# Kernel tuning notes

Hardware: AMD Instinct MI355X
Metric: run time of the kernel (lower is better)

Reference implementation:

```python
import jax, jax.numpy as jnp
import numpy as np

H, W = 480, 640
B = 4
P = 10          # number of accumulated flow passes (num_flows = 1)
N = 400000      # events per batch element
TREF = 1.0
TS_SCALING = 1.0
SPAT_W = 1.0
TEMP_W = 1.0


def _corners(loc):
    """loc: [M,2] (y,x) float -> flattened corner idx [4M] int32, bilinear weights [4M].
    Corner order: TL, TR, BL, BR (blocks of M), matching pol_mask repeat(1,4,1) layout.
    Out-of-grid corners get zero weight; indices are clamped in-range."""
    ty = jnp.floor(loc[:, 0:1])
    lx = jnp.floor(loc[:, 1:2])
    cs = jnp.concatenate([
        jnp.concatenate([ty, lx], 1),
        jnp.concatenate([ty, lx + 1.0], 1),
        jnp.concatenate([ty + 1.0, lx], 1),
        jnp.concatenate([ty + 1.0, lx + 1.0], 1)], axis=0)  # [4M,2]
    w = jnp.maximum(0.0, 1.0 - jnp.abs(jnp.tile(loc, (4, 1)) - cs))
    weights = w[:, 0] * w[:, 1]
    inb = ((cs[:, 0] >= 0) & (cs[:, 0] <= H - 1) &
           (cs[:, 1] >= 0) & (cs[:, 1] <= W - 1))
    weights = weights * inb.astype(weights.dtype)
    idx = (jnp.clip(cs[:, 0], 0, H - 1) * W + jnp.clip(cs[:, 1], 0, W - 1)).astype(jnp.int32)
    return idx, weights


def setup_inputs() -> dict:
    key = jax.random.key(0)
    k1, k2, k3, k4, k5 = jax.random.split(key, 5)
    scale = jnp.array([H - 1.0, W - 1.0], dtype=jnp.float32)
    warped_events = jax.random.uniform(k1, (B, N, 2), dtype=jnp.float32) * scale
    pos = jax.random.bernoulli(k2, 0.5, (B, N)).astype(jnp.float32)
    pos4 = jnp.tile(pos, (1, 4))                                   # [B,4N]
    pol_mask = jnp.stack([pos4, 1.0 - pos4], axis=-1)              # [B,4N,2]
    ts = jax.random.uniform(k3, (B, N, 1), dtype=jnp.float32)
    ts_list = jnp.tile(ts, (1, 4, 1))                              # [B,4N,1]
    flow_x = jax.random.normal(k4, (B, P, H, W), dtype=jnp.float32) * 3.0
    flow_y = jax.random.normal(k5, (B, P, H, W), dtype=jnp.float32) * 3.0
    return {"warped_events": warped_events, "pol_mask": pol_mask,
            "ts_list": ts_list, "flow_x": flow_x, "flow_y": flow_y}


def reference(warped_events, pol_mask, ts_list, flow_x, flow_y):
    f32 = flow_x.dtype
    # ---- iwe_formatting: bilinear scatter-add of warped events ----
    idx, weights = jax.vmap(_corners)(warped_events)               # [B,4N], [B,4N]
    norm_ts = 1.0 - jnp.abs(TREF - ts_list[..., 0]) / TS_SCALING   # [B,4N]

    def scat(i, w):
        return jnp.zeros(H * W, w.dtype).at[i].add(w)

    def img(w):
        return jax.vmap(scat)(idx, w).reshape(B, 1, H, W)

    iwe = jnp.concatenate([img(weights * pol_mask[:, :, 0]),
                           img(weights * pol_mask[:, :, 1])], axis=1)          # [B,2,H,W]
    iwe_ts = jnp.concatenate([img(weights * norm_ts * pol_mask[:, :, 0]),
                              img(weights * norm_ts * pol_mask[:, :, 1])], axis=1)

    # ---- focus_loss ----
    ts2 = iwe_ts.reshape(B, 2, -1)
    fl = jnp.sum(ts2[:, 0] ** 2, axis=1) + jnp.sum(ts2[:, 1] ** 2, axis=1)
    nz = (jnp.sum(iwe, axis=1) != 0).reshape(B, -1)
    fl = fl / (jnp.sum(nz, axis=1) + 1e-9)
    focus = jnp.sum(fl)

    # ---- flow_temporal_smoothing: warp grid by flow[j], gather flow[j+1] ----
    grid = jnp.stack(jnp.meshgrid(jnp.arange(H, dtype=f32),
                                  jnp.arange(W, dtype=f32), indexing='ij'), 0)  # [2,H,W] (y,x)
    flow = jnp.stack([flow_y[:, :-1], flow_x[:, :-1]], axis=2)                  # [B,P-1,2,H,W]
    loc = (grid[None, None] + flow).reshape(B, P - 1, 2, H * W).transpose(0, 1, 3, 2)  # [B,P-1,HW,2]
    m = ((loc[..., 0] >= 0) & (loc[..., 0] <= H - 1) &
         (loc[..., 1] >= 0) & (loc[..., 1] <= W - 1)).astype(f32)

    def samp(fx, fy, l):
        # fx, fy: [H,W]; l: [HW,2] -> sampled (y,x) flow [HW,2]
        i, w = _corners(l)
        sx = (fx.reshape(-1)[i] * w).reshape(4, -1).sum(0)
        sy = (fy.reshape(-1)[i] * w).reshape(4, -1).sum(0)
        return jnp.stack([sy, sx], axis=-1)

    wf = jax.vmap(jax.vmap(samp))(flow_x[:, 1:], flow_y[:, 1:], loc)            # [B,P-1,HW,2]
    ff = flow.reshape(B, P - 1, 2, H * W).transpose(0, 1, 3, 2)
    dt = jnp.sum(jnp.sqrt((ff - wf) ** 2 + 1e-9), axis=-1)                      # [B,P-1,HW]
    lt = jnp.sum(dt * m, axis=-1) / (jnp.sum(m, axis=-1) + 1e-9)                # [B,P-1]
    temporal = TEMP_W * jnp.sum(jnp.sum(lt, axis=1) / (P - 1))                  # num_flows = 1

    # ---- flow_spatial_smoothing: Charbonnier on 4 neighbor directions ----
    def charb(a):
        return jnp.sqrt(a ** 2 + 1e-6)

    dx = charb(flow_x[..., :-1] - flow_x[..., 1:]) + charb(flow_y[..., :-1] - flow_y[..., 1:])
    dy = charb(flow_x[:, :, :-1, :] - flow_x[:, :, 1:, :]) + charb(flow_y[:, :, :-1, :] - flow_y[:, :, 1:, :])
    ddr = charb(flow_x[:, :, :-1, :-1] - flow_x[:, :, 1:, 1:]) + charb(flow_y[:, :, :-1, :-1] - flow_y[:, :, 1:, 1:])
    dur = charb(flow_x[:, :, 1:, :-1] - flow_x[:, :, :-1, 1:]) + charb(flow_y[:, :, 1:, :-1] - flow_y[:, :, :-1, 1:])
    mm = lambda t: t.reshape(B, P, -1).mean(2).mean(1)
    spatial = SPAT_W * jnp.sum((mm(dx) + mm(dy) + mm(ddr) + mm(dur)) / 4.0)

    return focus + temporal + spatial
```

## Files before the change

### kernel.cpp

```cpp
#include <hip/hip_runtime.h>

#define BB 4
#define PP 10
#define NN 400000
#define HH 480
#define WW 640
constexpr int HW    = HH * WW;
constexpr int NXB   = HW / 256;
constexpr int TLW   = 64, TLH = 16;
constexpr int NXT   = (WW / TLW) * (HH / TLH);
constexpr int NTILE = NXT * BB * PP;
constexpr int CHUNK = NTILE / 8;
constexpr int EVB   = (BB * NN + NTILE - 1) / NTILE;

constexpr int WR = 41, WC = 89, WCP = 90;

constexpr int QW = WW / 2, QH = HH / 2, QN = QW * QH;
constexpr size_t IMG_QUADS = (size_t)4 * BB * 2 * QN;

constexpr float SCALE     = 1024.0f;
constexpr float INV_SCALE = 1.0f / 1024.0f;

constexpr int PF_V = 0;
constexpr int PF_N = PF_V + BB * NXB;
constexpr int PT_D = PF_N + BB * NXB;
constexpr int PT_M = PT_D + BB * (PP-1) * NXT * 4;
constexpr int PS   = PT_M + BB * (PP-1) * NXT * 4;
constexpr int NPART = PS + BB * PP * NXT * 4;


__device__ __forceinline__ float fsq(float a) { return __builtin_amdgcn_sqrtf(a); }
__device__ __forceinline__ float charb(float a) { return fsq(fmaf(a, a, 1e-6f)); }

__device__ __forceinline__ void waveSum3(float& a, float& b, float& c) {
    #pragma unroll
    for (int off = 32; off > 0; off >>= 1) {
        a += __shfl_down(a, off, 64);
        b += __shfl_down(b, off, 64);
        c += __shfl_down(c, off, 64);
    }
}

__device__ __forceinline__ float blockSum256(float v, float* smem) {
    #pragma unroll
    for (int off = 32; off > 0; off >>= 1)
        v += __shfl_down(v, off, 64);
    int lane = threadIdx.x & 63;
    int wid  = threadIdx.x >> 6;
    if (lane == 0) smem[wid] = v;
    __syncthreads();
    float r = 0.f;
    if (threadIdx.x == 0) r = smem[0] + smem[1] + smem[2] + smem[3];
    __syncthreads();
    return r;
}

__device__ __forceinline__ void scatter_one(int e,
                                            const float2* __restrict__ we,
                                            const float* __restrict__ pol,
                                            const float* __restrict__ tsl,
                                            unsigned long long* __restrict__ img) {
    int b = e / NN;
    int m = e - b * NN;
    float2 c = we[e];
    float y = c.x, x = c.y;
    float pm0 = pol[((size_t)b * 4 * NN + m) * 2];
    float ts  = tsl[(size_t)b * 4 * NN + m];
    float nts = 1.0f - fabsf(1.0f - ts);
    float tyf = fminf(fmaxf(floorf(y), 0.f), (float)(HH - 2));
    float lxf = fminf(fmaxf(floorf(x), 0.f), (float)(WW - 2));
    float fy_ = y - tyf, fx_ = x - lxf;
    float gy = 1.f - fy_, gx = 1.f - fx_;
    float s = nts * SCALE;
    unsigned long long wTL = (unsigned int)(gy * gx * s + 0.5f);
    unsigned long long wTR = (unsigned int)(gy * fx_ * s + 0.5f);
    unsigned long long wBL = (unsigned int)(fy_ * gx * s + 0.5f);
    unsigned long long wBR = (unsigned int)(fy_ * fx_ * s + 0.5f);
    unsigned long long val = wTL | (wTR << 16) | (wBL << 32) | (wBR << 48);
    int ty = (int)tyf, lx = (int)lxf;
    int pi = ((ty & 1) << 1) | (lx & 1);
    int pl = (pm0 > 0.5f) ? 0 : 1;
    size_t wi = ((size_t)((pi * BB + b) * 2 + pl)) * QN + (ty >> 1) * QW + (lx >> 1);
    atomicAdd(&img[wi], val);
}


__global__ __launch_bounds__(256)
void fused_kernel(const float2* __restrict__ we,
                  const float* __restrict__ pol,
                  const float* __restrict__ tsl,
                  const float* __restrict__ FX, const float* __restrict__ FY,
                  unsigned long long* __restrict__ img,
                  float* __restrict__ part) {
    __shared__ float sfx[WR][WCP];
    __shared__ float sfy[WR][WCP];
    int w = blockIdx.x;
    int t = threadIdx.x;

    int l  = (w & 7) * CHUNK + (w >> 3);
    int bp = l / NXT;
    int xb = l - bp * NXT;
    int b2 = bp / PP;
    int j  = bp - b2 * PP;
    int x0 = (xb % (WW / TLW)) * TLW;
    int y0 = (xb / (WW / TLW)) * TLH;
    const float* fx = FX + (size_t)bp * HW;
    const float* fy = FY + (size_t)bp * HW;
    const float* gx1 = fx + HW;
    const float* gy1 = fy + HW;
    bool hasT = (j < PP - 1);

    int wy0 = y0 - 12, wx0 = x0 - 12;
    if (hasT) {
        for (int idx = t; idx < WR * WC; idx += 256) {
            int r = idx / WC, c = idx - r * WC;
            int gy = min(max(wy0 + r, 0), HH - 1);
            int gc = min(max(wx0 + c, 0), WW - 1);
            sfx[r][c] = gx1[gy * WW + gc];
            sfy[r][c] = gy1[gy * WW + gc];
        }
    }

    int ypx = y0 + (t >> 4);
    int xpx = x0 + (t & 15) * 4;
    int p0  = ypx * WW + xpx;
    float4 vx = *(const float4*)(fx + p0);
    float4 vy = *(const float4*)(fy + p0);
    bool yin  = (ypx + 1 < HH);
    bool xend = (xpx == WW - 4);
    float4 bx4 = make_float4(0.f, 0.f, 0.f, 0.f), by4 = bx4;
    float vxr = 0.f, vyr = 0.f, bxr = 0.f, byr = 0.f;
    if (yin) {
        bx4 = *(const float4*)(fx + p0 + WW);
        by4 = *(const float4*)(fy + p0 + WW);
    }
    if (!xend) { vxr = fx[p0 + 4]; vyr = fy[p0 + 4]; }
    if (yin && !xend) { bxr = fx[p0 + WW + 4]; byr = fy[p0 + WW + 4]; }

    constexpr float cdx = 1.0f / ((float)HH * (WW - 1) * 4.0f * PP);
    constexpr float cdy = 1.0f / ((float)(HH - 1) * WW * 4.0f * PP);
    constexpr float cdd = 1.0f / ((float)(HH - 1) * (WW - 1) * 4.0f * PP);

    float acc = 0.f;
    acc += (charb(vx.x - vx.y) + charb(vy.x - vy.y)) * cdx;
    acc += (charb(vx.y - vx.z) + charb(vy.y - vy.z)) * cdx;
    acc += (charb(vx.z - vx.w) + charb(vy.z - vy.w)) * cdx;
    if (!xend) acc += (charb(vx.w - vxr) + charb(vy.w - vyr)) * cdx;
    if (yin) {
        acc += (charb(vx.x - bx4.x) + charb(vy.x - by4.x)) * cdy;
        acc += (charb(vx.y - bx4.y) + charb(vy.y - by4.y)) * cdy;
        acc += (charb(vx.z - bx4.z) + charb(vy.z - by4.z)) * cdy;
        acc += (charb(vx.w - bx4.w) + charb(vy.w - by4.w)) * cdy;
        acc += (charb(vx.x - bx4.y) + charb(vy.x - by4.y)) * cdd;
        acc += (charb(vx.y - bx4.z) + charb(vy.y - by4.z)) * cdd;
        acc += (charb(vx.z - bx4.w) + charb(vy.z - by4.w)) * cdd;
        acc += (charb(bx4.x - vx.y) + charb(by4.x - vy.y)) * cdd;
        acc += (charb(bx4.y - vx.z) + charb(by4.y - vy.z)) * cdd;
        acc += (charb(bx4.z - vx.w) + charb(by4.z - vy.w)) * cdd;
        if (!xend) {
            acc += (charb(vx.w - bxr) + charb(vy.w - byr)) * cdd;
            acc += (charb(bx4.w - vxr) + charb(by4.w - vyr)) * cdd;
        }
    }

    float td = 0.f, tm = 0.f;
    if (hasT) {
        __syncthreads();
        float ax[4] = {vx.x, vx.y, vx.z, vx.w};
        float ay[4] = {vy.x, vy.y, vy.z, vy.w};
        #pragma unroll
        for (int i = 0; i < 4; ++i) {
            float ly  = (float)ypx + ay[i];
            float lx2 = (float)(xpx + i) + ax[i];
            bool m = (ly >= 0.f) && (ly <= (float)(HH - 1)) &&
                     (lx2 >= 0.f) && (lx2 <= (float)(WW - 1));
            if (m) {
                tm += 1.f;
                float tyf = fminf(fmaxf(floorf(ly),  0.f), (float)(HH - 2));
                float txf = fminf(fmaxf(floorf(lx2), 0.f), (float)(WW - 2));
                int ity = (int)tyf, itx = (int)txf;
                float fyy = ly - tyf, fxx = lx2 - txf;
                float gyy = 1.f - fyy, gxx = 1.f - fxx;
                float x00, x01, x10, x11, y00, y01, y10, y11;
                if (ity >= wy0 && ity <= wy0 + WR - 2 &&
                    itx >= wx0 && itx <= wx0 + WC - 2) {
                    int r = ity - wy0, c = itx - wx0;
                    x00 = sfx[r][c];     x01 = sfx[r][c + 1];
                    x10 = sfx[r + 1][c]; x11 = sfx[r + 1][c + 1];
                    y00 = sfy[r][c];     y01 = sfy[r][c + 1];
                    y10 = sfy[r + 1][c]; y11 = sfy[r + 1][c + 1];
                } else {
                    int pix = ity * WW + itx;
                    x00 = gx1[pix];      x01 = gx1[pix + 1];
                    x10 = gx1[pix + WW]; x11 = gx1[pix + WW + 1];
                    y00 = gy1[pix];      y01 = gy1[pix + 1];
                    y10 = gy1[pix + WW]; y11 = gy1[pix + WW + 1];
                }
                float sx = gyy * (gxx * x00 + fxx * x01) + fyy * (gxx * x10 + fxx * x11);
                float sy = gyy * (gxx * y00 + fxx * y01) + fyy * (gxx * y10 + fxx * y11);
                float dy_ = ay[i] - sy;
                float dx_ = ax[i] - sx;
                td += fsq(fmaf(dy_, dy_, 1e-9f)) + fsq(fmaf(dx_, dx_, 1e-9f));
            }
        }
    }

    __builtin_amdgcn_sched_barrier(0);
    int e = w * EVB + t;
    if (t < EVB && e < BB * NN)
        scatter_one(e, we, pol, tsl, img);
    __builtin_amdgcn_sched_barrier(0);

    waveSum3(acc, td, tm);
    if ((t & 63) == 0) {
        int wid = t >> 6;
        part[PS + (bp * NXT + xb) * 4 + wid] = acc;
        if (hasT) {
            int bj = b2 * (PP - 1) + j;
            part[PT_D + (bj * NXT + xb) * 4 + wid] = td;
            part[PT_M + (bj * NXT + xb) * 4 + wid] = tm;
        }
    }
}


__global__ __launch_bounds__(256)
void focus_kernel(const unsigned long long* __restrict__ img,
                  float* __restrict__ part) {
    __shared__ float sm[8];
    int b = blockIdx.y;
    int p = blockIdx.x * 256 + threadIdx.x;
    int y = p / WW;
    int x = p - y * WW;
    unsigned int sp = 0, sn = 0;
    #pragma unroll
    for (int dy = 0; dy < 2; ++dy) {
        #pragma unroll
        for (int dx = 0; dx < 2; ++dx) {
            int ty = y - dy, lx = x - dx;
            if (ty < 0 || lx < 0 || ty > HH - 2 || lx > WW - 2) continue;
            int pi = ((ty & 1) << 1) | (lx & 1);
            size_t base = ((size_t)(pi * BB + b) * 2) * QN + (ty >> 1) * QW + (lx >> 1);
            int sh = 16 * ((dy << 1) | dx);
            sp += (unsigned int)((img[base]      >> sh) & 0xFFFFull);
            sn += (unsigned int)((img[base + QN] >> sh) & 0xFFFFull);
        }
    }
    float tp = (float)sp * INV_SCALE;
    float tn = (float)sn * INV_SCALE;
    float v  = tp * tp + tn * tn;
    float nz = ((sp | sn) != 0u) ? 1.f : 0.f;
    float sv  = blockSum256(v, sm);
    float snz = blockSum256(nz, sm + 4);
    if (threadIdx.x == 0) {
        part[PF_V + b * NXB + blockIdx.x] = sv;
        part[PF_N + b * NXB + blockIdx.x] = snz;
    }
}


__global__ __launch_bounds__(256)
void reduce_kernel(const float* __restrict__ part, float* __restrict__ seg) {
    __shared__ float sm[4];
    int s = blockIdx.x;
    int base, len;
    if (s < 4)       { base = PF_V + s * NXB;            len = NXB; }
    else if (s < 8)  { base = PF_N + (s - 4) * NXB;      len = NXB; }
    else if (s < 44) { base = PT_D + (s - 8) * NXT * 4;  len = NXT * 4; }
    else if (s < 80) { base = PT_M + (s - 44) * NXT * 4; len = NXT * 4; }
    else             { base = PS;                        len = BB * PP * NXT * 4; }
    float v = 0.f;
    for (int i = threadIdx.x; i < len; i += 256) v += part[base + i];
    float r = blockSum256(v, sm);
    if (threadIdx.x == 0) seg[s] = r;
}


__global__ void final_kernel(const float* __restrict__ seg, float* __restrict__ out) {
    if (threadIdx.x == 0 && blockIdx.x == 0) {
        float focus = 0.f;
        #pragma unroll
        for (int b = 0; b < BB; ++b)
            focus += seg[b] / (seg[BB + b] + 1e-9f);
        float temporal = 0.f;
        #pragma unroll
        for (int k = 0; k < BB * (PP - 1); ++k)
            temporal += seg[8 + k] / (seg[44 + k] + 1e-9f);
        temporal *= 1.0f / (float)(PP - 1);
        out[0] = focus + temporal + seg[80];
    }
}


extern "C" void kernel_launch(void* const* d_in, const int* in_sizes, int n_in,
                              void* d_out, int out_size, void* d_ws, size_t ws_size,
                              hipStream_t stream) {
    const float2* we  = (const float2*)d_in[0];
    const float*  pol = (const float*)d_in[1];
    const float*  tsl = (const float*)d_in[2];
    const float*  FX  = (const float*)d_in[3];
    const float*  FY  = (const float*)d_in[4];
    float*              seg  = (float*)d_ws;
    unsigned long long* img  = (unsigned long long*)(seg + 256);
    float*              part = (float*)(img + IMG_QUADS);

    hipMemsetAsync(img, 0, IMG_QUADS * sizeof(unsigned long long), stream);

    fused_kernel<<<NTILE, 256, 0, stream>>>(we, pol, tsl, FX, FY, img, part);
    focus_kernel<<<dim3(NXB, BB), 256, 0, stream>>>(img, part);
    reduce_kernel<<<81, 256, 0, stream>>>(part, seg);
    final_kernel<<<1, 64, 0, stream>>>(seg, (float*)d_out);
}
```

Measured before the change: 180.3 us.

## Add a dedicated scatter wave and interleave the flow window in shared memory

Launches the fused kernel with a fifth wavefront that handles all of a tile's event scatter atomics. Each lane of that wave processes three events and issues their loads before the block barrier. The four compute waves no longer run the scatter themselves. The warped-flow shared window now stores x and y interleaved as float2, so each bilinear corner is one LDS read instead of two. The halo shrinks from 12 to 10 pixels, so more samples may fall back to global loads. The block barrier is now unconditional so the scatter wave and the compute waves meet at it.

```diff
diff --git a/kernel.cpp b/kernel.cpp
--- a/kernel.cpp
+++ b/kernel.cpp
@@ -13,7 +13,7 @@
 constexpr int CHUNK = NTILE / 8;
 constexpr int EVB   = (BB * NN + NTILE - 1) / NTILE;
 
-constexpr int WR = 41, WC = 89, WCP = 90;
+constexpr int WR = 37, WC = 85;
 
 constexpr int QW = WW / 2, QH = HH / 2, QN = QW * QH;
 constexpr size_t IMG_QUADS = (size_t)4 * BB * 2 * QN;
@@ -55,45 +55,15 @@
     return r;
 }
 
-__device__ __forceinline__ void scatter_one(int e,
-                                            const float2* __restrict__ we,
-                                            const float* __restrict__ pol,
-                                            const float* __restrict__ tsl,
-                                            unsigned long long* __restrict__ img) {
-    int b = e / NN;
-    int m = e - b * NN;
-    float2 c = we[e];
-    float y = c.x, x = c.y;
-    float pm0 = pol[((size_t)b * 4 * NN + m) * 2];
-    float ts  = tsl[(size_t)b * 4 * NN + m];
-    float nts = 1.0f - fabsf(1.0f - ts);
-    float tyf = fminf(fmaxf(floorf(y), 0.f), (float)(HH - 2));
-    float lxf = fminf(fmaxf(floorf(x), 0.f), (float)(WW - 2));
-    float fy_ = y - tyf, fx_ = x - lxf;
-    float gy = 1.f - fy_, gx = 1.f - fx_;
-    float s = nts * SCALE;
-    unsigned long long wTL = (unsigned int)(gy * gx * s + 0.5f);
-    unsigned long long wTR = (unsigned int)(gy * fx_ * s + 0.5f);
-    unsigned long long wBL = (unsigned int)(fy_ * gx * s + 0.5f);
-    unsigned long long wBR = (unsigned int)(fy_ * fx_ * s + 0.5f);
-    unsigned long long val = wTL | (wTR << 16) | (wBL << 32) | (wBR << 48);
-    int ty = (int)tyf, lx = (int)lxf;
-    int pi = ((ty & 1) << 1) | (lx & 1);
-    int pl = (pm0 > 0.5f) ? 0 : 1;
-    size_t wi = ((size_t)((pi * BB + b) * 2 + pl)) * QN + (ty >> 1) * QW + (lx >> 1);
-    atomicAdd(&img[wi], val);
-}
-
-
-__global__ __launch_bounds__(256)
+
+__global__ __launch_bounds__(320)
 void fused_kernel(const float2* __restrict__ we,
                   const float* __restrict__ pol,
                   const float* __restrict__ tsl,
                   const float* __restrict__ FX, const float* __restrict__ FY,
                   unsigned long long* __restrict__ img,
                   float* __restrict__ part) {
-    __shared__ float sfx[WR][WCP];
-    __shared__ float sfy[WR][WCP];
+    __shared__ float2 sxy[WR][WC];
     int w = blockIdx.x;
     int t = threadIdx.x;
 
@@ -109,15 +79,60 @@
     const float* gx1 = fx + HW;
     const float* gy1 = fy + HW;
     bool hasT = (j < PP - 1);
-
-    int wy0 = y0 - 12, wx0 = x0 - 12;
+    int wy0 = y0 - 10, wx0 = x0 - 10;
+
+    if (t >= 256) {
+        int ln = t - 256;
+        int e0 = w * EVB + ln;
+        int e1 = e0 + 64, e2 = e1 + 64;
+        bool v0 = (ln      < EVB) && (e0 < BB * NN);
+        bool v1 = (ln + 64 < EVB) && (e1 < BB * NN);
+        bool v2 = (ln + 128 < EVB) && (e2 < BB * NN);
+        float2 c0 = {0,0}, c1 = {0,0}, c2 = {0,0};
+        float pm0 = 0, pm1 = 0, pm2 = 0, t0 = 0, t1 = 0, t2 = 0;
+        int b0i = 0, b1i = 0, b2i = 0;
+        if (v0) { b0i = e0 / NN; int m = e0 - b0i * NN; c0 = we[e0];
+                  pm0 = pol[((size_t)b0i * 4 * NN + m) * 2]; t0 = tsl[(size_t)b0i * 4 * NN + m]; }
+        if (v1) { b1i = e1 / NN; int m = e1 - b1i * NN; c1 = we[e1];
+                  pm1 = pol[((size_t)b1i * 4 * NN + m) * 2]; t1 = tsl[(size_t)b1i * 4 * NN + m]; }
+        if (v2) { b2i = e2 / NN; int m = e2 - b2i * NN; c2 = we[e2];
+                  pm2 = pol[((size_t)b2i * 4 * NN + m) * 2]; t2 = tsl[(size_t)b2i * 4 * NN + m]; }
+        __syncthreads();
+        #define DO_SCAT(vv, cc, pm, ts, bi)                                          \
+        if (vv) {                                                                    \
+            float y = cc.x, x = cc.y;                                                \
+            float nts = 1.0f - fabsf(1.0f - (ts));                                   \
+            float tyf = fminf(fmaxf(floorf(y), 0.f), (float)(HH - 2));               \
+            float lxf = fminf(fmaxf(floorf(x), 0.f), (float)(WW - 2));               \
+            float fy_ = y - tyf, fx_ = x - lxf;                                      \
+            float gy = 1.f - fy_, gxw = 1.f - fx_;                                   \
+            float s = nts * SCALE;                                                   \
+            unsigned long long wTL = (unsigned int)(gy * gxw * s + 0.5f);            \
+            unsigned long long wTR = (unsigned int)(gy * fx_ * s + 0.5f);            \
+            unsigned long long wBL = (unsigned int)(fy_ * gxw * s + 0.5f);           \
+            unsigned long long wBR = (unsigned int)(fy_ * fx_ * s + 0.5f);           \
+            unsigned long long val = wTL | (wTR << 16) | (wBL << 32) | (wBR << 48);  \
+            int ty = (int)tyf, lxq = (int)lxf;                                       \
+            int pi = ((ty & 1) << 1) | (lxq & 1);                                    \
+            int pl = ((pm) > 0.5f) ? 0 : 1;                                          \
+            size_t wi = ((size_t)((pi * BB + (bi)) * 2 + pl)) * QN                   \
+                        + (ty >> 1) * QW + (lxq >> 1);                               \
+            atomicAdd(&img[wi], val);                                                \
+        }
+        DO_SCAT(v0, c0, pm0, t0, b0i)
+        DO_SCAT(v1, c1, pm1, t1, b1i)
+        DO_SCAT(v2, c2, pm2, t2, b2i)
+        #undef DO_SCAT
+        return;
+    }
+
     if (hasT) {
         for (int idx = t; idx < WR * WC; idx += 256) {
             int r = idx / WC, c = idx - r * WC;
             int gy = min(max(wy0 + r, 0), HH - 1);
             int gc = min(max(wx0 + c, 0), WW - 1);
-            sfx[r][c] = gx1[gy * WW + gc];
-            sfy[r][c] = gy1[gy * WW + gc];
+            int g  = gy * WW + gc;
+            sxy[r][c] = make_float2(gx1[g], gy1[g]);
         }
     }
 
@@ -163,9 +178,10 @@
         }
     }
 
+    __syncthreads();
+
     float td = 0.f, tm = 0.f;
     if (hasT) {
-        __syncthreads();
         float ax[4] = {vx.x, vx.y, vx.z, vx.w};
         float ay[4] = {vy.x, vy.y, vy.z, vy.w};
         #pragma unroll
@@ -181,35 +197,27 @@
                 int ity = (int)tyf, itx = (int)txf;
                 float fyy = ly - tyf, fxx = lx2 - txf;
                 float gyy = 1.f - fyy, gxx = 1.f - fxx;
-                float x00, x01, x10, x11, y00, y01, y10, y11;
+                float2 q00, q01, q10, q11;
                 if (ity >= wy0 && ity <= wy0 + WR - 2 &&
                     itx >= wx0 && itx <= wx0 + WC - 2) {
                     int r = ity - wy0, c = itx - wx0;
-                    x00 = sfx[r][c];     x01 = sfx[r][c + 1];
-                    x10 = sfx[r + 1][c]; x11 = sfx[r + 1][c + 1];
-                    y00 = sfy[r][c];     y01 = sfy[r][c + 1];
-                    y10 = sfy[r + 1][c]; y11 = sfy[r + 1][c + 1];
+                    q00 = sxy[r][c];     q01 = sxy[r][c + 1];
+                    q10 = sxy[r + 1][c]; q11 = sxy[r + 1][c + 1];
                 } else {
                     int pix = ity * WW + itx;
-                    x00 = gx1[pix];      x01 = gx1[pix + 1];
-                    x10 = gx1[pix + WW]; x11 = gx1[pix + WW + 1];
-                    y00 = gy1[pix];      y01 = gy1[pix + 1];
-                    y10 = gy1[pix + WW]; y11 = gy1[pix + WW + 1];
+                    q00 = make_float2(gx1[pix],          gy1[pix]);
+                    q01 = make_float2(gx1[pix + 1],      gy1[pix + 1]);
+                    q10 = make_float2(gx1[pix + WW],     gy1[pix + WW]);
+                    q11 = make_float2(gx1[pix + WW + 1], gy1[pix + WW + 1]);
                 }
-                float sx = gyy * (gxx * x00 + fxx * x01) + fyy * (gxx * x10 + fxx * x11);
-                float sy = gyy * (gxx * y00 + fxx * y01) + fyy * (gxx * y10 + fxx * y11);
+                float sx = gyy * (gxx * q00.x + fxx * q01.x) + fyy * (gxx * q10.x + fxx * q11.x);
+                float sy = gyy * (gxx * q00.y + fxx * q01.y) + fyy * (gxx * q10.y + fxx * q11.y);
                 float dy_ = ay[i] - sy;
                 float dx_ = ax[i] - sx;
                 td += fsq(fmaf(dy_, dy_, 1e-9f)) + fsq(fmaf(dx_, dx_, 1e-9f));
             }
         }
     }
-
-    __builtin_amdgcn_sched_barrier(0);
-    int e = w * EVB + t;
-    if (t < EVB && e < BB * NN)
-        scatter_one(e, we, pol, tsl, img);
-    __builtin_amdgcn_sched_barrier(0);
 
     waveSum3(acc, td, tm);
     if ((t & 63) == 0) {
@@ -306,7 +314,7 @@
 
     hipMemsetAsync(img, 0, IMG_QUADS * sizeof(unsigned long long), stream);
 
-    fused_kernel<<<NTILE, 256, 0, stream>>>(we, pol, tsl, FX, FY, img, part);
+    fused_kernel<<<NTILE, 320, 0, stream>>>(we, pol, tsl, FX, FY, img, part);
     focus_kernel<<<dim3(NXB, BB), 256, 0, stream>>>(img, part);
     reduce_kernel<<<81, 256, 0, stream>>>(part, seg);
     final_kernel<<<1, 64, 0, stream>>>(seg, (float*)d_out);
```

Measured after the change: 171.6 us. -4.8%, faster.

## Split event scatter into dedicated blocks and interleave with flow tiles

Applied to the files above, without the earlier changes.

Instead of every flow tile block scattering a handful of events (EVB per block), one block in every 13 now scatters a contiguous chunk of 1600 events while the other 12 handle flow tiles. The shared-memory halo for the temporal warp shrinks from 12 to 8 pixels, and the x/y flow values are stored interleaved as float2 so each corner is one LDS load. The aim is to reduce per-block tail work and the shared-memory footprint, which may raise occupancy. The trade-offs are more global fallback loads when a warped location falls outside the smaller halo, and an unconditional __syncthreads that now also runs in non-temporal blocks.

```diff
diff --git a/kernel.cpp b/kernel.cpp
--- a/kernel.cpp
+++ b/kernel.cpp
@@ -11,9 +11,10 @@
 constexpr int NXT   = (WW / TLW) * (HH / TLH);
 constexpr int NTILE = NXT * BB * PP;
 constexpr int CHUNK = NTILE / 8;
-constexpr int EVB   = (BB * NN + NTILE - 1) / NTILE;
-
-constexpr int WR = 41, WC = 89, WCP = 90;
+constexpr int NGRP  = 1000;
+constexpr int EVS   = BB * NN / NGRP;
+
+constexpr int WR = 33, WC = 81;
 
 constexpr int QW = WW / 2, QH = HH / 2, QN = QW * QH;
 constexpr size_t IMG_QUADS = (size_t)4 * BB * 2 * QN;
@@ -92,12 +93,21 @@
                   const float* __restrict__ FX, const float* __restrict__ FY,
                   unsigned long long* __restrict__ img,
                   float* __restrict__ part) {
-    __shared__ float sfx[WR][WCP];
-    __shared__ float sfy[WR][WCP];
+    __shared__ float2 sxy[WR][WC];
     int w = blockIdx.x;
     int t = threadIdx.x;
-
-    int l  = (w & 7) * CHUNK + (w >> 3);
+    int group = w / 13;
+    int pos   = w - group * 13;
+
+    if (pos == 12) {
+        int base = group * EVS;
+        for (int k = t; k < EVS; k += 256)
+            scatter_one(base + k, we, pol, tsl, img);
+        return;
+    }
+
+    int fidx = group * 12 + pos;
+    int l  = (fidx & 7) * CHUNK + (fidx >> 3);
     int bp = l / NXT;
     int xb = l - bp * NXT;
     int b2 = bp / PP;
@@ -109,15 +119,15 @@
     const float* gx1 = fx + HW;
     const float* gy1 = fy + HW;
     bool hasT = (j < PP - 1);
-
-    int wy0 = y0 - 12, wx0 = x0 - 12;
+    int wy0 = y0 - 8, wx0 = x0 - 8;
+
     if (hasT) {
         for (int idx = t; idx < WR * WC; idx += 256) {
             int r = idx / WC, c = idx - r * WC;
             int gy = min(max(wy0 + r, 0), HH - 1);
             int gc = min(max(wx0 + c, 0), WW - 1);
-            sfx[r][c] = gx1[gy * WW + gc];
-            sfy[r][c] = gy1[gy * WW + gc];
+            int g  = gy * WW + gc;
+            sxy[r][c] = make_float2(gx1[g], gy1[g]);
         }
     }
 
@@ -163,9 +173,10 @@
         }
     }
 
+    __syncthreads();
+
     float td = 0.f, tm = 0.f;
     if (hasT) {
-        __syncthreads();
         float ax[4] = {vx.x, vx.y, vx.z, vx.w};
         float ay[4] = {vy.x, vy.y, vy.z, vy.w};
         #pragma unroll
@@ -181,35 +192,27 @@
                 int ity = (int)tyf, itx = (int)txf;
                 float fyy = ly - tyf, fxx = lx2 - txf;
                 float gyy = 1.f - fyy, gxx = 1.f - fxx;
-                float x00, x01, x10, x11, y00, y01, y10, y11;
+                float2 q00, q01, q10, q11;
                 if (ity >= wy0 && ity <= wy0 + WR - 2 &&
                     itx >= wx0 && itx <= wx0 + WC - 2) {
                     int r = ity - wy0, c = itx - wx0;
-                    x00 = sfx[r][c];     x01 = sfx[r][c + 1];
-                    x10 = sfx[r + 1][c]; x11 = sfx[r + 1][c + 1];
-                    y00 = sfy[r][c];     y01 = sfy[r][c + 1];
-                    y10 = sfy[r + 1][c]; y11 = sfy[r + 1][c + 1];
+                    q00 = sxy[r][c];     q01 = sxy[r][c + 1];
+                    q10 = sxy[r + 1][c]; q11 = sxy[r + 1][c + 1];
                 } else {
                     int pix = ity * WW + itx;
-                    x00 = gx1[pix];      x01 = gx1[pix + 1];
-                    x10 = gx1[pix + WW]; x11 = gx1[pix + WW + 1];
-                    y00 = gy1[pix];      y01 = gy1[pix + 1];
-                    y10 = gy1[pix + WW]; y11 = gy1[pix + WW + 1];
+                    q00 = make_float2(gx1[pix],          gy1[pix]);
+                    q01 = make_float2(gx1[pix + 1],      gy1[pix + 1]);
+                    q10 = make_float2(gx1[pix + WW],     gy1[pix + WW]);
+                    q11 = make_float2(gx1[pix + WW + 1], gy1[pix + WW + 1]);
                 }
-                float sx = gyy * (gxx * x00 + fxx * x01) + fyy * (gxx * x10 + fxx * x11);
-                float sy = gyy * (gxx * y00 + fxx * y01) + fyy * (gxx * y10 + fxx * y11);
+                float sx = gyy * (gxx * q00.x + fxx * q01.x) + fyy * (gxx * q10.x + fxx * q11.x);
+                float sy = gyy * (gxx * q00.y + fxx * q01.y) + fyy * (gxx * q10.y + fxx * q11.y);
                 float dy_ = ay[i] - sy;
                 float dx_ = ax[i] - sx;
                 td += fsq(fmaf(dy_, dy_, 1e-9f)) + fsq(fmaf(dx_, dx_, 1e-9f));
             }
         }
     }
-
-    __builtin_amdgcn_sched_barrier(0);
-    int e = w * EVB + t;
-    if (t < EVB && e < BB * NN)
-        scatter_one(e, we, pol, tsl, img);
-    __builtin_amdgcn_sched_barrier(0);
 
     waveSum3(acc, td, tm);
     if ((t & 63) == 0) {
@@ -306,7 +309,7 @@
 
     hipMemsetAsync(img, 0, IMG_QUADS * sizeof(unsigned long long), stream);
 
-    fused_kernel<<<NTILE, 256, 0, stream>>>(we, pol, tsl, FX, FY, img, part);
+    fused_kernel<<<NGRP * 13, 256, 0, stream>>>(we, pol, tsl, FX, FY, img, part);
     focus_kernel<<<dim3(NXB, BB), 256, 0, stream>>>(img, part);
     reduce_kernel<<<81, 256, 0, stream>>>(part, seg);
     final_kernel<<<1, 64, 0, stream>>>(seg, (float*)d_out);
```

New measurement: 160.0 us. -11.3%, faster.
